# Optimization experiments

Measured on AMD Instinct MI355X. Metric: run time of the kernel, lower is better.

The kernel has to match this reference:

```python
import jax, jax.numpy as jnp
import numpy as np

B, K, N, D, H, DOUT = 16, 8, 196, 768, 3072, 768


def setup_inputs() -> dict:
    key = jax.random.key(0)
    ks = jax.random.split(key, 5)
    scale_w1 = 1.0 / np.sqrt(D)
    scale_w2 = 1.0 / np.sqrt(H)
    return {
        "slots": jax.random.normal(ks[0], (B, K, D), dtype=jnp.float32),
        "pos_embed": jax.random.normal(ks[1], (N, D), dtype=jnp.float32) * 0.02,
        "map_alpha": jax.random.normal(ks[2], (N, DOUT), dtype=jnp.float32) * 0.02,
        "W1": jax.random.normal(ks[3], (D, H), dtype=jnp.float32) * scale_w1,
        "b1": jnp.zeros((H,), dtype=jnp.float32),
        "W2": jax.random.normal(ks[4], (H, DOUT), dtype=jnp.float32) * scale_w2,
        "b2": jnp.zeros((DOUT,), dtype=jnp.float32),
    }


def reference(slots, pos_embed, map_alpha, W1, b1, W2, b2):
    b, k, d = slots.shape
    n = pos_embed.shape[0]
    # broadcast slots over patches and add positional embedding: (B,K,N,D)
    tokens = slots[:, :, None, :] + pos_embed[None, None, :, :]
    # 2-layer MLP with ReLU
    h = jax.nn.relu(jnp.einsum('bknd,dh->bknh', tokens, W1) + b1)
    y_k = jnp.einsum('bknh,ho->bkno', h, W2) + b2  # (B,K,N,DOUT)
    # softmax over K of map_alpha expanded over (B,K); identical across K -> uniform 1/K,
    # computed explicitly for faithfulness to the original module
    m_k = jax.nn.softmax(jnp.broadcast_to(map_alpha[None, None, :, :], (b, k, n, map_alpha.shape[1])), axis=1)
    y = jnp.einsum('bknd,bknd->bnd', y_k, m_k)
    return y
```

## Files before the change

### kernel.cpp

```cpp
#include <hip/hip_runtime.h>
#include <hip/hip_bf16.h>
#include <stdint.h>


typedef __attribute__((ext_vector_type(8))) short bf16x8;
typedef __attribute__((ext_vector_type(4))) float f32x4;

#define AS1 __attribute__((address_space(1)))
#define AS3 __attribute__((address_space(3)))

#define WAIT_VM(N) asm volatile("s_waitcnt vmcnt(" #N ")" ::: "memory")
#define BAR()      asm volatile("s_barrier" ::: "memory")
#define BAR_LDS()  asm volatile("s_waitcnt lgkmcnt(0)\ns_barrier" ::: "memory")

static __device__ __forceinline__ void gld_lds16(const void* g, void* l) {
    __builtin_amdgcn_global_load_lds((const AS1 unsigned int*)g,
                                     (AS3 unsigned int*)l, 16, 0, 0);
}

static __device__ __forceinline__ unsigned short f2bf(float f) {
    union { float f; unsigned int u; } v; v.f = f;
    unsigned int u = v.u;
    return (unsigned short)((u + 0x7fffu + ((u >> 16) & 1u)) >> 16);
}

static __device__ __forceinline__ void conv_tiled(const float* __restrict__ W,
                                                  unsigned short* __restrict__ Wt,
                                                  int Kd, int Rd, int idx) {
    int r  = idx % Rd;
    int kc = idx / Rd;
    unsigned int po[4];
    #pragma unroll
    for (int j = 0; j < 4; ++j) {
        unsigned short lo = f2bf(W[(size_t)(kc * 8 + 2 * j) * Rd + r]);
        unsigned short hi = f2bf(W[(size_t)(kc * 8 + 2 * j + 1) * Rd + r]);
        po[j] = (unsigned int)lo | ((unsigned int)hi << 16);
    }
    size_t dst = ((size_t)(r >> 6) * (Kd >> 6) + (kc >> 3)) * 4096
               + (size_t)((kc & 7) * 64 + (r & 63)) * 8;
    *(uint4*)(Wt + dst) = make_uint4(po[0], po[1], po[2], po[3]);
}

__global__ void k_prep(const float* __restrict__ W1, unsigned short* __restrict__ W1t,
                       const float* __restrict__ W2, unsigned short* __restrict__ W2t,
                       const float* __restrict__ S, const float* __restrict__ P,
                       unsigned short* __restrict__ A1) {
    int idx = blockIdx.x * blockDim.x + threadIdx.x;
    const int C1n = 96 * 3072;
    const int C2n = 384 * 768;
    const int PKn = 96 * 384;
    if (idx < C1n) {
        conv_tiled(W1, W1t, 768, 3072, idx);
    } else if (idx < C1n + C2n) {
        conv_tiled(W2, W2t, 3072, 768, idx - C1n);
    } else if (idx < C1n + C2n + PKn) {
        int t = idx - C1n - C2n;
        int r  = t % 384;
        int kc = t / 384;
        uint4 o = make_uint4(0u, 0u, 0u, 0u);
        if (r < 324) {
            const float* src = (r < 128) ? (S + (size_t)r * 768 + kc * 8)
                                         : (P + (size_t)(r - 128) * 768 + kc * 8);
            float4 a = *(const float4*)(src);
            float4 b = *(const float4*)(src + 4);
            o.x = (unsigned int)f2bf(a.x) | ((unsigned int)f2bf(a.y) << 16);
            o.y = (unsigned int)f2bf(a.z) | ((unsigned int)f2bf(a.w) << 16);
            o.z = (unsigned int)f2bf(b.x) | ((unsigned int)f2bf(b.y) << 16);
            o.w = (unsigned int)f2bf(b.z) | ((unsigned int)f2bf(b.w) << 16);
        }
        size_t dst = ((size_t)(r >> 6) * 12 + (kc >> 3)) * 4096
                   + (size_t)((kc & 7) * 64 + (r & 63)) * 8;
        *(uint4*)(A1 + dst) = o;
    }
}

__global__ void k_hbar(const float* __restrict__ C1, const float* __restrict__ b1,
                       unsigned short* __restrict__ Hb) {
    const int lane = threadIdx.x & 63;
    const int wv   = threadIdx.x >> 6;
    const int hc   = blockIdx.y * 4 + wv;
    const int h0   = hc * 8;
    const int bn   = blockIdx.x * 64 + lane;
    const int b    = bn / 196;
    const int n    = bn - b * 196;
    const float* prow = C1 + (size_t)(128 + n) * 3072 + h0;
    float4 pA = *(const float4*)(prow);
    float4 pB = *(const float4*)(prow + 4);
    float4 bA = *(const float4*)(b1 + h0);
    float4 bB = *(const float4*)(b1 + h0 + 4);
    float pb[8] = { pA.x + bA.x, pA.y + bA.y, pA.z + bA.z, pA.w + bA.w,
                    pB.x + bB.x, pB.y + bB.y, pB.z + bB.z, pB.w + bB.w };
    float acc[8] = {};
    #pragma unroll
    for (int k = 0; k < 8; ++k) {
        const float* srow = C1 + (size_t)(b * 8 + k) * 3072 + h0;
        float4 sA_ = *(const float4*)(srow);
        float4 sB_ = *(const float4*)(srow + 4);
        acc[0] += fmaxf(sA_.x + pb[0], 0.f);
        acc[1] += fmaxf(sA_.y + pb[1], 0.f);
        acc[2] += fmaxf(sA_.z + pb[2], 0.f);
        acc[3] += fmaxf(sA_.w + pb[3], 0.f);
        acc[4] += fmaxf(sB_.x + pb[4], 0.f);
        acc[5] += fmaxf(sB_.y + pb[5], 0.f);
        acc[6] += fmaxf(sB_.z + pb[6], 0.f);
        acc[7] += fmaxf(sB_.w + pb[7], 0.f);
    }
    unsigned int w0 = (unsigned int)f2bf(acc[0] * 0.125f) | ((unsigned int)f2bf(acc[1] * 0.125f) << 16);
    unsigned int w1 = (unsigned int)f2bf(acc[2] * 0.125f) | ((unsigned int)f2bf(acc[3] * 0.125f) << 16);
    unsigned int w2 = (unsigned int)f2bf(acc[4] * 0.125f) | ((unsigned int)f2bf(acc[5] * 0.125f) << 16);
    unsigned int w3 = (unsigned int)f2bf(acc[6] * 0.125f) | ((unsigned int)f2bf(acc[7] * 0.125f) << 16);
    size_t dst = ((size_t)blockIdx.x * 48 + (hc >> 3)) * 4096
               + (size_t)((hc & 7) * 64 + lane) * 8;
    *(uint4*)(Hb + dst) = make_uint4(w0, w1, w2, w3);
}

__launch_bounds__(256)
__global__ void gemm_tiled(const unsigned short* __restrict__ A,
                           const unsigned short* __restrict__ Bt,
                           const float* __restrict__ bias,
                           float* __restrict__ C,
                           int Mstore, int Nd, int KT) {
    __shared__ unsigned short sm[3 * 8192];

    const int tid  = threadIdx.x;
    const int lane = tid & 63;
    const int wave = tid >> 6;
    const int wm = wave >> 1, wn = wave & 1;
    const int q = lane >> 4, l16 = lane & 15;

    const unsigned short* Ab = A  + (size_t)blockIdx.y * KT * 4096;
    const unsigned short* Bb = Bt + (size_t)blockIdx.x * KT * 4096;

    f32x4 acc[2][2] = {};

    const int offA = (wm * 32 + l16) * 8;
    const int offB = 4096 + (wn * 32 + l16) * 8;

    auto stage = [&](int i, unsigned short* d) {
        const unsigned short* Ag = Ab + (size_t)i * 4096;
        const unsigned short* Bg = Bb + (size_t)i * 4096;
        gld_lds16(Ag + tid * 8,        d + tid * 8);
        gld_lds16(Ag + 2048 + tid * 8, d + 2048 + tid * 8);
        gld_lds16(Bg + tid * 8,        d + 4096 + tid * 8);
        gld_lds16(Bg + 2048 + tid * 8, d + 6144 + tid * 8);
    };
    auto compute = [&](const unsigned short* buf) {
        #pragma unroll
        for (int ks = 0; ks < 2; ++ks) {
            const int ko = (ks * 4 + q) * 512;
            bf16x8 af0 = *(const bf16x8*)(buf + ko + offA);
            bf16x8 af1 = *(const bf16x8*)(buf + ko + offA + 128);
            bf16x8 bf0 = *(const bf16x8*)(buf + ko + offB);
            bf16x8 bf1 = *(const bf16x8*)(buf + ko + offB + 128);
            acc[0][0] = __builtin_amdgcn_mfma_f32_16x16x32_bf16(af0, bf0, acc[0][0], 0, 0, 0);
            acc[0][1] = __builtin_amdgcn_mfma_f32_16x16x32_bf16(af0, bf1, acc[0][1], 0, 0, 0);
            acc[1][0] = __builtin_amdgcn_mfma_f32_16x16x32_bf16(af1, bf0, acc[1][0], 0, 0, 0);
            acc[1][1] = __builtin_amdgcn_mfma_f32_16x16x32_bf16(af1, bf1, acc[1][1], 0, 0, 0);
        }
    };

    unsigned short* b0 = sm;
    unsigned short* b1 = sm + 8192;
    unsigned short* b2 = sm + 16384;

    stage(0, b0);
    stage(1, b1);
    for (int i = 0; i < KT; i += 3) {
        stage(i + 2, b2); WAIT_VM(8);
        BAR();
        compute(b0);
        BAR_LDS();
        if (i + 3 < KT) { stage(i + 3, b0); WAIT_VM(8); } else { WAIT_VM(4); }
        BAR();
        compute(b1);
        BAR_LDS();
        if (i + 4 < KT) { stage(i + 4, b1); WAIT_VM(8); }
        else if (i + 3 < KT) { WAIT_VM(4); }
        else { WAIT_VM(0); }
        BAR();
        compute(b2);
        if (i + 3 < KT) BAR_LDS();
    }

    const int row0 = blockIdx.y * 64 + wm * 32;
    const int col0 = blockIdx.x * 64 + wn * 32;
    #pragma unroll
    for (int ii = 0; ii < 2; ++ii) {
        #pragma unroll
        for (int jj = 0; jj < 2; ++jj) {
            int col = col0 + jj * 16 + l16;
            float bv = bias ? bias[col] : 0.f;
            #pragma unroll
            for (int r = 0; r < 4; ++r) {
                int row = row0 + ii * 16 + q * 4 + r;
                if (row < Mstore) C[(size_t)row * Nd + col] = acc[ii][jj][r] + bv;
            }
        }
    }
}

extern "C" void kernel_launch(void* const* d_in, const int* in_sizes, int n_in,
                              void* d_out, int out_size, void* d_ws, size_t ws_size,
                              hipStream_t stream) {
    const float* slots  = (const float*)d_in[0];
    const float* pos    = (const float*)d_in[1];
    const float* W1     = (const float*)d_in[3];
    const float* b1     = (const float*)d_in[4];
    const float* W2     = (const float*)d_in[5];
    const float* b2     = (const float*)d_in[6];
    float* out = (float*)d_out;

    size_t off = 0;
    auto alloc = [&](size_t bytes) {
        void* p = (char*)d_ws + off;
        off += (bytes + 255) & ~(size_t)255;
        return p;
    };
    unsigned short* W1t = (unsigned short*)alloc((size_t)3072 * 768 * 2);
    unsigned short* W2t = (unsigned short*)alloc((size_t)768 * 3072 * 2);
    unsigned short* A1  = (unsigned short*)alloc((size_t)384 * 768 * 2);
    float*          C1  = (float*)alloc((size_t)384 * 3072 * 4);
    unsigned short* Hb  = (unsigned short*)alloc((size_t)3136 * 3072 * 2);

    k_prep<<<2448, 256, 0, stream>>>(W1, W1t, W2, W2t, slots, pos, A1);
    gemm_tiled<<<dim3(48, 6), 256, 0, stream>>>(A1, W1t, nullptr, C1, 324, 3072, 12);
    k_hbar<<<dim3(49, 96), 256, 0, stream>>>(C1, b1, Hb);
    gemm_tiled<<<dim3(12, 49), 256, 0, stream>>>(Hb, W2t, b2, out, 3136, 768, 48);
}
```

Before: 137.3 us.

## Move W2 conversion into hbar kernel, enlarge GEMM2 tiles, remap block order

Moves the W2 bf16 conversion out of the prep kernel and into the hbar kernel as extra blocks, so the first GEMM no longer waits for it. The second GEMM becomes a dedicated 512-thread kernel with 128x64 tiles and a grouped block ordering meant to improve L2 reuse of Hb and W2t and reduce tail blocks. GEMM1 also gets a remapped 1D block order, and Hb is padded to 50 row tiles so the last tile is fully written. The cost is more LDS per block and a tail of 12 blocks in GEMM2 that repeat the partial last row tile.

```diff
diff --git a/kernel.cpp b/kernel.cpp
--- a/kernel.cpp
+++ b/kernel.cpp
@@ -24,37 +24,27 @@
     return (unsigned short)((u + 0x7fffu + ((u >> 16) & 1u)) >> 16);
 }
 
-static __device__ __forceinline__ void conv_tiled(const float* __restrict__ W,
-                                                  unsigned short* __restrict__ Wt,
-                                                  int Kd, int Rd, int idx) {
-    int r  = idx % Rd;
-    int kc = idx / Rd;
-    unsigned int po[4];
-    #pragma unroll
-    for (int j = 0; j < 4; ++j) {
-        unsigned short lo = f2bf(W[(size_t)(kc * 8 + 2 * j) * Rd + r]);
-        unsigned short hi = f2bf(W[(size_t)(kc * 8 + 2 * j + 1) * Rd + r]);
-        po[j] = (unsigned int)lo | ((unsigned int)hi << 16);
-    }
-    size_t dst = ((size_t)(r >> 6) * (Kd >> 6) + (kc >> 3)) * 4096
-               + (size_t)((kc & 7) * 64 + (r & 63)) * 8;
-    *(uint4*)(Wt + dst) = make_uint4(po[0], po[1], po[2], po[3]);
-}
-
 __global__ void k_prep(const float* __restrict__ W1, unsigned short* __restrict__ W1t,
-                       const float* __restrict__ W2, unsigned short* __restrict__ W2t,
                        const float* __restrict__ S, const float* __restrict__ P,
                        unsigned short* __restrict__ A1) {
     int idx = blockIdx.x * blockDim.x + threadIdx.x;
     const int C1n = 96 * 3072;
-    const int C2n = 384 * 768;
     const int PKn = 96 * 384;
     if (idx < C1n) {
-        conv_tiled(W1, W1t, 768, 3072, idx);
-    } else if (idx < C1n + C2n) {
-        conv_tiled(W2, W2t, 3072, 768, idx - C1n);
-    } else if (idx < C1n + C2n + PKn) {
-        int t = idx - C1n - C2n;
+        int r  = idx % 3072;
+        int kc = idx / 3072;
+        unsigned int po[4];
+        #pragma unroll
+        for (int j = 0; j < 4; ++j) {
+            unsigned short lo = f2bf(W1[(size_t)(kc * 8 + 2 * j) * 3072 + r]);
+            unsigned short hi = f2bf(W1[(size_t)(kc * 8 + 2 * j + 1) * 3072 + r]);
+            po[j] = (unsigned int)lo | ((unsigned int)hi << 16);
+        }
+        size_t dst = ((size_t)(r >> 6) * 12 + (kc >> 3)) * 4096
+                   + (size_t)((kc & 7) * 64 + (r & 63)) * 8;
+        *(uint4*)(W1t + dst) = make_uint4(po[0], po[1], po[2], po[3]);
+    } else if (idx < C1n + PKn) {
+        int t = idx - C1n;
         int r  = t % 384;
         int kc = t / 384;
         uint4 o = make_uint4(0u, 0u, 0u, 0u);
@@ -74,15 +64,37 @@
     }
 }
 
-__global__ void k_hbar(const float* __restrict__ C1, const float* __restrict__ b1,
-                       unsigned short* __restrict__ Hb) {
-    const int lane = threadIdx.x & 63;
-    const int wv   = threadIdx.x >> 6;
-    const int hc   = blockIdx.y * 4 + wv;
+__global__ void k_hbar_w2t(const float* __restrict__ C1, const float* __restrict__ b1,
+                           unsigned short* __restrict__ Hb,
+                           const float* __restrict__ W2, unsigned short* __restrict__ W2t) {
+    const int bid = blockIdx.x;
+    const int tid = threadIdx.x;
+    if (bid >= 4800) {
+        int idx = (bid - 4800) * 256 + tid;
+        int r  = idx % 768;
+        int kc = idx / 768;
+        unsigned int po[4];
+        #pragma unroll
+        for (int j = 0; j < 4; ++j) {
+            unsigned short lo = f2bf(W2[(size_t)(kc * 8 + 2 * j) * 768 + r]);
+            unsigned short hi = f2bf(W2[(size_t)(kc * 8 + 2 * j + 1) * 768 + r]);
+            po[j] = (unsigned int)lo | ((unsigned int)hi << 16);
+        }
+        size_t dst = ((size_t)(r >> 6) * 48 + (kc >> 3)) * 4096
+                   + (size_t)((kc & 7) * 64 + (r & 63)) * 8;
+        *(uint4*)(W2t + dst) = make_uint4(po[0], po[1], po[2], po[3]);
+        return;
+    }
+    const int bx   = bid % 50;
+    const int yq   = bid / 50;
+    const int lane = tid & 63;
+    const int wv   = tid >> 6;
+    const int hc   = yq * 4 + wv;
     const int h0   = hc * 8;
-    const int bn   = blockIdx.x * 64 + lane;
-    const int b    = bn / 196;
-    const int n    = bn - b * 196;
+    int bn = bx * 64 + lane;
+    if (bn > 3135) bn = 3135;
+    const int b = bn / 196;
+    const int n = bn - b * 196;
     const float* prow = C1 + (size_t)(128 + n) * 3072 + h0;
     float4 pA = *(const float4*)(prow);
     float4 pB = *(const float4*)(prow + 4);
@@ -109,7 +121,7 @@
     unsigned int w1 = (unsigned int)f2bf(acc[2] * 0.125f) | ((unsigned int)f2bf(acc[3] * 0.125f) << 16);
     unsigned int w2 = (unsigned int)f2bf(acc[4] * 0.125f) | ((unsigned int)f2bf(acc[5] * 0.125f) << 16);
     unsigned int w3 = (unsigned int)f2bf(acc[6] * 0.125f) | ((unsigned int)f2bf(acc[7] * 0.125f) << 16);
-    size_t dst = ((size_t)blockIdx.x * 48 + (hc >> 3)) * 4096
+    size_t dst = ((size_t)bx * 48 + (hc >> 3)) * 4096
                + (size_t)((hc & 7) * 64 + lane) * 8;
     *(uint4*)(Hb + dst) = make_uint4(w0, w1, w2, w3);
 }
@@ -117,7 +129,6 @@
 __launch_bounds__(256)
 __global__ void gemm_tiled(const unsigned short* __restrict__ A,
                            const unsigned short* __restrict__ Bt,
-                           const float* __restrict__ bias,
                            float* __restrict__ C,
                            int Mstore, int Nd, int KT) {
     __shared__ unsigned short sm[3 * 8192];
@@ -128,11 +139,15 @@
     const int wm = wave >> 1, wn = wave & 1;
     const int q = lane >> 4, l16 = lane & 15;
 
-    const unsigned short* Ab = A  + (size_t)blockIdx.y * KT * 4096;
-    const unsigned short* Bb = Bt + (size_t)blockIdx.x * KT * 4096;
+    const int id = blockIdx.x;
+    const int j  = id >> 3;
+    const int nt = (id & 7) * 6 + j % 6;
+    const int rt = j / 6;
+
+    const unsigned short* Ab = A  + (size_t)rt * KT * 4096;
+    const unsigned short* Bb = Bt + (size_t)nt * KT * 4096;
 
     f32x4 acc[2][2] = {};
-
     const int offA = (wm * 32 + l16) * 8;
     const int offB = 4096 + (wn * 32 + l16) * 8;
 
@@ -159,41 +174,120 @@
         }
     };
 
-    unsigned short* b0 = sm;
-    unsigned short* b1 = sm + 8192;
-    unsigned short* b2 = sm + 16384;
-
-    stage(0, b0);
-    stage(1, b1);
+    unsigned short* s0 = sm;
+    unsigned short* s1 = sm + 8192;
+    unsigned short* s2 = sm + 16384;
+
+    stage(0, s0);
+    stage(1, s1);
     for (int i = 0; i < KT; i += 3) {
-        stage(i + 2, b2); WAIT_VM(8);
-        BAR();
-        compute(b0);
-        BAR_LDS();
-        if (i + 3 < KT) { stage(i + 3, b0); WAIT_VM(8); } else { WAIT_VM(4); }
-        BAR();
-        compute(b1);
-        BAR_LDS();
-        if (i + 4 < KT) { stage(i + 4, b1); WAIT_VM(8); }
+        stage(i + 2, s2); WAIT_VM(8);
+        BAR(); compute(s0); BAR_LDS();
+        if (i + 3 < KT) { stage(i + 3, s0); WAIT_VM(8); } else { WAIT_VM(4); }
+        BAR(); compute(s1); BAR_LDS();
+        if (i + 4 < KT) { stage(i + 4, s1); WAIT_VM(8); }
         else if (i + 3 < KT) { WAIT_VM(4); }
         else { WAIT_VM(0); }
-        BAR();
-        compute(b2);
+        BAR(); compute(s2);
         if (i + 3 < KT) BAR_LDS();
     }
 
-    const int row0 = blockIdx.y * 64 + wm * 32;
-    const int col0 = blockIdx.x * 64 + wn * 32;
+    const int row0 = rt * 64 + wm * 32;
+    const int col0 = nt * 64 + wn * 32;
     #pragma unroll
     for (int ii = 0; ii < 2; ++ii) {
         #pragma unroll
         for (int jj = 0; jj < 2; ++jj) {
             int col = col0 + jj * 16 + l16;
-            float bv = bias ? bias[col] : 0.f;
             #pragma unroll
             for (int r = 0; r < 4; ++r) {
                 int row = row0 + ii * 16 + q * 4 + r;
-                if (row < Mstore) C[(size_t)row * Nd + col] = acc[ii][jj][r] + bv;
+                if (row < Mstore) C[(size_t)row * Nd + col] = acc[ii][jj][r];
+            }
+        }
+    }
+}
+
+__launch_bounds__(512)
+__global__ void k_gemm2(const unsigned short* __restrict__ Hb,
+                        const unsigned short* __restrict__ W2t,
+                        const float* __restrict__ b2, float* __restrict__ out) {
+    __shared__ unsigned short sm[3 * 12288];
+
+    const int tid  = threadIdx.x;
+    const int lane = tid & 63;
+    const int wave = tid >> 6;
+    const int wm = wave >> 1, wn = wave & 1;
+    const int q = lane >> 4, l16 = lane & 15;
+
+    const int id = blockIdx.x;
+    int rt, nt;
+    if (id < 288) { rt = (id / 96) * 8 + (id & 7); nt = (id % 96) >> 3; }
+    else          { rt = 24; nt = id - 288; }
+
+    const unsigned short* A0b = Hb  + ((size_t)(2 * rt)     * 48) * 4096;
+    const unsigned short* A1b = Hb  + ((size_t)(2 * rt + 1) * 48) * 4096;
+    const unsigned short* Bb  = W2t + ((size_t)nt * 48) * 4096;
+
+    f32x4 acc[2][2] = {};
+
+    auto stage = [&](int i, unsigned short* d) {
+        gld_lds16(A0b + (size_t)i * 4096 + tid * 8, d + tid * 8);
+        gld_lds16(A1b + (size_t)i * 4096 + tid * 8, d + 4096 + tid * 8);
+        gld_lds16(Bb  + (size_t)i * 4096 + tid * 8, d + 8192 + tid * 8);
+    };
+
+    const int r0 = wm * 32 + l16;
+    const int aoff0 = (r0 >> 6) * 4096 + (r0 & 63) * 8;
+    const int r1 = wm * 32 + 16 + l16;
+    const int aoff1 = (r1 >> 6) * 4096 + (r1 & 63) * 8;
+    const int boff  = 8192 + (wn * 32 + l16) * 8;
+
+    auto compute = [&](const unsigned short* buf) {
+        #pragma unroll
+        for (int ks = 0; ks < 2; ++ks) {
+            const int ko = (ks * 4 + q) * 512;
+            bf16x8 af0 = *(const bf16x8*)(buf + aoff0 + ko);
+            bf16x8 af1 = *(const bf16x8*)(buf + aoff1 + ko);
+            bf16x8 bf0 = *(const bf16x8*)(buf + boff + ko);
+            bf16x8 bf1 = *(const bf16x8*)(buf + boff + ko + 128);
+            acc[0][0] = __builtin_amdgcn_mfma_f32_16x16x32_bf16(af0, bf0, acc[0][0], 0, 0, 0);
+            acc[0][1] = __builtin_amdgcn_mfma_f32_16x16x32_bf16(af0, bf1, acc[0][1], 0, 0, 0);
+            acc[1][0] = __builtin_amdgcn_mfma_f32_16x16x32_bf16(af1, bf0, acc[1][0], 0, 0, 0);
+            acc[1][1] = __builtin_amdgcn_mfma_f32_16x16x32_bf16(af1, bf1, acc[1][1], 0, 0, 0);
+        }
+    };
+
+    unsigned short* s0 = sm;
+    unsigned short* s1 = sm + 12288;
+    unsigned short* s2 = sm + 24576;
+
+    stage(0, s0);
+    stage(1, s1);
+    for (int i = 0; i < 48; i += 3) {
+        stage(i + 2, s2); WAIT_VM(6);
+        BAR(); compute(s0); BAR_LDS();
+        if (i + 3 < 48) { stage(i + 3, s0); WAIT_VM(6); } else { WAIT_VM(3); }
+        BAR(); compute(s1); BAR_LDS();
+        if (i + 4 < 48) { stage(i + 4, s1); WAIT_VM(6); }
+        else if (i + 3 < 48) { WAIT_VM(3); }
+        else { WAIT_VM(0); }
+        BAR(); compute(s2);
+        if (i + 3 < 48) BAR_LDS();
+    }
+
+    const int row0 = rt * 128 + wm * 32;
+    const int col0 = nt * 64 + wn * 32;
+    #pragma unroll
+    for (int ii = 0; ii < 2; ++ii) {
+        #pragma unroll
+        for (int jj = 0; jj < 2; ++jj) {
+            int col = col0 + jj * 16 + l16;
+            float bv = b2[col];
+            #pragma unroll
+            for (int r = 0; r < 4; ++r) {
+                int row = row0 + ii * 16 + q * 4 + r;
+                if (row < 3136) out[(size_t)row * 768 + col] = acc[ii][jj][r] + bv;
             }
         }
     }
@@ -220,10 +314,10 @@
     unsigned short* W2t = (unsigned short*)alloc((size_t)768 * 3072 * 2);
     unsigned short* A1  = (unsigned short*)alloc((size_t)384 * 768 * 2);
     float*          C1  = (float*)alloc((size_t)384 * 3072 * 4);
-    unsigned short* Hb  = (unsigned short*)alloc((size_t)3136 * 3072 * 2);
-
-    k_prep<<<2448, 256, 0, stream>>>(W1, W1t, W2, W2t, slots, pos, A1);
-    gemm_tiled<<<dim3(48, 6), 256, 0, stream>>>(A1, W1t, nullptr, C1, 324, 3072, 12);
-    k_hbar<<<dim3(49, 96), 256, 0, stream>>>(C1, b1, Hb);
-    gemm_tiled<<<dim3(12, 49), 256, 0, stream>>>(Hb, W2t, b2, out, 3136, 768, 48);
-}
+    unsigned short* Hb  = (unsigned short*)alloc((size_t)50 * 48 * 4096 * 2);
+
+    k_prep<<<1296, 256, 0, stream>>>(W1, W1t, slots, pos, A1);
+    gemm_tiled<<<288, 256, 0, stream>>>(A1, W1t, C1, 324, 3072, 12);
+    k_hbar_w2t<<<5952, 256, 0, stream>>>(C1, b1, Hb, W2, W2t);
+    k_gemm2<<<300, 512, 0, stream>>>(Hb, W2t, b2, out);
+}
```

Result: faster. 129.9 us (-5.4%).
